# Performance work log

Hardware: AMD Instinct MI355X
Metric: run time of the kernel (lower is better)

Reference implementation:

```python
import jax, jax.numpy as jnp
import numpy as np

KSIZE = 9
SIGMA = 7.0
ALPHA = 0.05
POOL = 7


def _conv(x, w, pad):
    # x: (N, Cin, H, W), w: (Cout, Cin, kh, kw), zero padding, stride 1
    return jax.lax.conv_general_dilated(
        x, w, window_strides=(1, 1), padding=[(pad, pad), (pad, pad)],
        dimension_numbers=("NCHW", "OIHW", "NCHW"))


def setup_inputs() -> dict:
    key = jax.random.key(0)
    x = jax.random.normal(key, (4, 1, 2048, 2048), dtype=jnp.float32)
    # Sobel filters (ImageGradientsLayer): out ch 0 = Ix, out ch 1 = Iy
    sobel_w = jnp.array(
        [[[[-1., 0., 1.], [-2., 0., 2.], [-1., 0., 1.]]],
         [[[-1., -2., -1.], [0., 0., 0.], [1., 2., 1.]]]], dtype=jnp.float32)
    # Normalized 2D Gaussian kernel, ksize=9, sigma=7
    ax = np.arange(KSIZE) - (KSIZE - 1) / 2.0
    g1 = np.exp(-(ax ** 2) / (2.0 * SIGMA ** 2))
    g2 = np.outer(g1, g1)
    g2 = g2 / g2.sum()
    gauss_w = jnp.asarray(g2, dtype=jnp.float32)[None, None]  # (1,1,9,9)
    return {"x": x, "sobel_w": sobel_w, "gauss_w": gauss_w}


def reference(x, sobel_w, gauss_w):
    # 1) ImageGradientsLayer: Sobel conv -> (N, 2, H, W)
    g = _conv(x, sobel_w, 1)
    Ix, Iy = g[:, 0], g[:, 1]
    # 2) ChannelProductLayer: I_xx, I_yy, I_xy -> (N, 3, H, W)
    prods = jnp.stack([Ix * Ix, Iy * Iy, Ix * Iy], axis=1)
    # 3) SecondMomentMatrixLayer: same 9x9 Gaussian on each channel
    N, C, H, W = prods.shape
    S = _conv(prods.reshape(N * C, 1, H, W), gauss_w, (KSIZE - 1) // 2)
    S = S.reshape(N, C, H, W)
    # 4) CornerResponseLayer: R = det - alpha * trace^2
    det = S[:, 0] * S[:, 1] - S[:, 2] * S[:, 2]
    tr = S[:, 0] + S[:, 1]
    R = (det - ALPHA * tr * tr)[:, None]  # (N, 1, H, W)
    # 5) NMSLayer: global (lower) median threshold, 7x7 maxpool, equality mask
    n = R.size
    med = jnp.sort(R.reshape(-1))[(n - 1) // 2]  # torch.median = lower median
    xt = jnp.where(R > med, R, jnp.zeros_like(R))
    pad = (POOL - 1) // 2
    y = jax.lax.reduce_window(
        xt, -jnp.inf, jax.lax.max, (1, 1, POOL, POOL), (1, 1, 1, 1),
        [(0, 0), (0, 0), (pad, pad), (pad, pad)])
    mask = (xt == y).astype(xt.dtype)
    return mask * xt
```

## Files before the change

kernel.cpp:

```cpp
#include <hip/hip_runtime.h>
#include <cstdint>
#include <math.h>

#define IMH 2048
#define IMW 2048
#define NB 4
#define NPIX (NB*IMH*IMW)
#define MEDRANK ((NPIX-1)/2)
#define ALPHA 0.05f

#define TW 64
#define TH 32

__device__ __forceinline__ uint32_t fkey(float f){
  uint32_t u = __float_as_uint(f);
  return (u & 0x80000000u) ? ~u : (u | 0x80000000u);
}

__device__ __forceinline__ float ldz(const float* __restrict__ p, int r, int c){
  return (r >= 0 && r < IMH && c >= 0 && c < IMW) ? p[(size_t)r*IMW + c] : 0.f;
}

__global__ __launch_bounds__(256) void front_kernel(
    const float* __restrict__ x, const float* __restrict__ sobel_w,
    const float* __restrict__ gauss_w, float* __restrict__ R)
{
  __shared__ float xs[TH+10][84];
  __shared__ float hs[3][TH+8][68];

  const int tid = threadIdx.x;
  const int C0 = blockIdx.x * TW;
  const int R0 = blockIdx.y * TH;
  const int n  = blockIdx.z;
  const float* xb = x + (size_t)n * (size_t)(IMH*IMW);

  float w0[9], w1[9];
#pragma unroll
  for (int i = 0; i < 9; i++){ w0[i] = sobel_w[i]; w1[i] = sobel_w[9+i]; }
  float ga[9];
  {
    float a4 = sqrtf(gauss_w[4*9+4]);
#pragma unroll
    for (int i = 0; i < 9; i++) ga[i] = gauss_w[4*9+i] / a4;
  }

  for (int u = tid; u < (TH+10)*20; u += 256){
    int r  = u / 20, c4 = u % 20;
    int gr = R0 - 5 + r;
    int gc = C0 - 8 + c4*4;
    float4 v;
    if (gr >= 0 && gr < IMH && gc >= 0 && gc + 3 < IMW){
      v = *reinterpret_cast<const float4*>(&xb[(size_t)gr*IMW + gc]);
    } else {
      v.x = ldz(xb, gr, gc+0);
      v.y = ldz(xb, gr, gc+1);
      v.z = ldz(xb, gr, gc+2);
      v.w = ldz(xb, gr, gc+3);
    }
    *reinterpret_cast<float4*>(&xs[r][c4*4]) = v;
  }
  __syncthreads();

  for (int u = tid; u < (TH+8)*16; u += 256){
    int hr = u >> 4;
    int oc = (u & 15) * 4;
    int gr = R0 - 4 + hr;
    bool rowv = ((unsigned)gr < (unsigned)IMH);

    float ix[12], iy[12];
#pragma unroll
    for (int j = 0; j < 12; j++){ ix[j] = 0.f; iy[j] = 0.f; }
#pragma unroll
    for (int i = 0; i < 3; i++){
      float xr[20];
#pragma unroll
      for (int m = 0; m < 5; m++){
        float4 t = *reinterpret_cast<const float4*>(&xs[hr+i][oc + m*4]);
        xr[m*4+0]=t.x; xr[m*4+1]=t.y; xr[m*4+2]=t.z; xr[m*4+3]=t.w;
      }
#pragma unroll
      for (int j = 0; j < 12; j++){
#pragma unroll
        for (int d = 0; d < 3; d++){
          float xv = xr[3 + j + d];
          ix[j] = fmaf(w0[i*3+d], xv, ix[j]);
          iy[j] = fmaf(w1[i*3+d], xv, iy[j]);
        }
      }
    }
    float pr[3][12];
#pragma unroll
    for (int j = 0; j < 12; j++){
      int gc = C0 + oc - 4 + j;
      bool v = rowv && ((unsigned)gc < (unsigned)IMW);
      float a = v ? ix[j] : 0.f;
      float b = v ? iy[j] : 0.f;
      pr[0][j] = a*a; pr[1][j] = b*b; pr[2][j] = a*b;
    }
#pragma unroll
    for (int p = 0; p < 3; p++){
      float o[4];
#pragma unroll
      for (int jj = 0; jj < 4; jj++){
        float s = 0.f;
#pragma unroll
        for (int k = 0; k < 9; k++) s = fmaf(ga[k], pr[p][jj+k], s);
        o[jj] = s;
      }
      *reinterpret_cast<float4*>(&hs[p][hr][oc]) = make_float4(o[0],o[1],o[2],o[3]);
    }
  }
  __syncthreads();

  const int c4o = tid & 15;
  const int r0o = (tid >> 4) * 2;
  float4 sA[3], sB[3];
#pragma unroll
  for (int p = 0; p < 3; p++){
    float4 a0 = make_float4(0,0,0,0), a1 = make_float4(0,0,0,0);
#pragma unroll
    for (int k = 0; k < 10; k++){
      float4 hv = *reinterpret_cast<const float4*>(&hs[p][r0o+k][c4o*4]);
      if (k < 9){
        a0.x = fmaf(ga[k], hv.x, a0.x); a0.y = fmaf(ga[k], hv.y, a0.y);
        a0.z = fmaf(ga[k], hv.z, a0.z); a0.w = fmaf(ga[k], hv.w, a0.w);
      }
      if (k >= 1){
        a1.x = fmaf(ga[k-1], hv.x, a1.x); a1.y = fmaf(ga[k-1], hv.y, a1.y);
        a1.z = fmaf(ga[k-1], hv.z, a1.z); a1.w = fmaf(ga[k-1], hv.w, a1.w);
      }
    }
    sA[p] = a0; sB[p] = a1;
  }

  float* Rb = R + (size_t)n * (size_t)(IMH*IMW);
  {
    float4 o0, o1;
    float s0, s1, s2, det, tr;
    s0=sA[0].x; s1=sA[1].x; s2=sA[2].x; det=s0*s1-s2*s2; tr=s0+s1; o0.x=det-ALPHA*tr*tr;
    s0=sA[0].y; s1=sA[1].y; s2=sA[2].y; det=s0*s1-s2*s2; tr=s0+s1; o0.y=det-ALPHA*tr*tr;
    s0=sA[0].z; s1=sA[1].z; s2=sA[2].z; det=s0*s1-s2*s2; tr=s0+s1; o0.z=det-ALPHA*tr*tr;
    s0=sA[0].w; s1=sA[1].w; s2=sA[2].w; det=s0*s1-s2*s2; tr=s0+s1; o0.w=det-ALPHA*tr*tr;
    s0=sB[0].x; s1=sB[1].x; s2=sB[2].x; det=s0*s1-s2*s2; tr=s0+s1; o1.x=det-ALPHA*tr*tr;
    s0=sB[0].y; s1=sB[1].y; s2=sB[2].y; det=s0*s1-s2*s2; tr=s0+s1; o1.y=det-ALPHA*tr*tr;
    s0=sB[0].z; s1=sB[1].z; s2=sB[2].z; det=s0*s1-s2*s2; tr=s0+s1; o1.z=det-ALPHA*tr*tr;
    s0=sB[0].w; s1=sB[1].w; s2=sB[2].w; det=s0*s1-s2*s2; tr=s0+s1; o1.w=det-ALPHA*tr*tr;

    int orow = R0 + r0o;
    int ocol = C0 + c4o*4;
    *reinterpret_cast<float4*>(&Rb[(size_t)orow*IMW + ocol])     = o0;
    *reinterpret_cast<float4*>(&Rb[(size_t)(orow+1)*IMW + ocol]) = o1;
  }
}

__global__ __launch_bounds__(256) void hist8_kernel(
    const float4* __restrict__ R4, uint32_t* __restrict__ h)
{
  __shared__ uint32_t lh[256*32];
  for (int i = threadIdx.x; i < 256*32; i += 256) lh[i] = 0;
  __syncthreads();
  const int copy = threadIdx.x & 31;
  const int stride = gridDim.x * 256;
  for (int i = blockIdx.x*256 + threadIdx.x; i < NPIX/4; i += stride){
    float4 v = R4[i];
    atomicAdd(&lh[(fkey(v.x) >> 24)*32 + copy], 1u);
    atomicAdd(&lh[(fkey(v.y) >> 24)*32 + copy], 1u);
    atomicAdd(&lh[(fkey(v.z) >> 24)*32 + copy], 1u);
    atomicAdd(&lh[(fkey(v.w) >> 24)*32 + copy], 1u);
  }
  __syncthreads();
  {
    const int t = threadIdx.x;
    uint32_t s = 0;
#pragma unroll
    for (int i = 0; i < 32; i++) s += lh[t*32 + ((t + i) & 31)];
    if (s) atomicAdd(&h[t], s);
  }
}

__global__ __launch_bounds__(256) void hist12_kernel(
    const float4* __restrict__ R4, uint32_t* __restrict__ h,
    const uint32_t* __restrict__ state, int phase)
{
  __shared__ uint32_t lh[4096];
  for (int i = threadIdx.x; i < 4096; i += 256) lh[i] = 0;
  __syncthreads();
  const uint32_t target = (phase == 0) ? state[0] : ((state[0] << 12) | state[2]);
  const int shift = (phase == 0) ? 24 : 12;
  const int stride = gridDim.x * 256;
  for (int i = blockIdx.x*256 + threadIdx.x; i < NPIX/4; i += stride){
    float4 v = R4[i];
    uint32_t k;
    k = fkey(v.x); if ((k >> shift) == target) atomicAdd(&lh[(k >> (shift-12)) & 0xfffu], 1u);
    k = fkey(v.y); if ((k >> shift) == target) atomicAdd(&lh[(k >> (shift-12)) & 0xfffu], 1u);
    k = fkey(v.z); if ((k >> shift) == target) atomicAdd(&lh[(k >> (shift-12)) & 0xfffu], 1u);
    k = fkey(v.w); if ((k >> shift) == target) atomicAdd(&lh[(k >> (shift-12)) & 0xfffu], 1u);
  }
  __syncthreads();
  for (int i = threadIdx.x; i < 4096; i += 256)
    if (lh[i]) atomicAdd(&h[i], lh[i]);
}

__global__ __launch_bounds__(256) void select_kernel(
    const uint32_t* __restrict__ h, uint32_t* __restrict__ state,
    int nbins, int phase)
{
  __shared__ uint32_t sc[256];
  const int t = threadIdx.x;
  const int chunk = nbins >> 8;
  uint32_t lsum = 0;
  for (int i = 0; i < chunk; i++) lsum += h[t*chunk + i];
  sc[t] = lsum;
  __syncthreads();
  for (int off = 1; off < 256; off <<= 1){
    uint32_t v = (t >= off) ? sc[t-off] : 0u;
    __syncthreads();
    sc[t] += v;
    __syncthreads();
  }
  const uint32_t excl = sc[t] - lsum;
  const uint32_t rank = (phase == 0) ? (uint32_t)MEDRANK : state[(phase == 1) ? 1 : 3];
  if (rank >= excl && rank < excl + lsum){
    uint32_t cum = excl;
    for (int i = 0; i < chunk; i++){
      uint32_t c = h[t*chunk + i];
      if (rank < cum + c){
        uint32_t bin = (uint32_t)(t*chunk + i);
        if (phase == 0){ state[0] = bin; state[1] = rank - cum; }
        else if (phase == 1){ state[2] = bin; state[3] = rank - cum; }
        else {
          uint32_t key = (state[0] << 24) | (state[2] << 12) | bin;
          uint32_t u = (key & 0x80000000u) ? (key & 0x7fffffffu) : ~key;
          state[4] = u;
        }
        break;
      }
      cum += c;
    }
  }
}

#define PT 64
__global__ __launch_bounds__(256) void nms_kernel(
    const float* __restrict__ R, const uint32_t* __restrict__ state,
    float* __restrict__ out)
{
  __shared__ float xt[PT+6][76];
  __shared__ float hm[PT+6][68];

  const int tid = threadIdx.x;
  const int C0 = blockIdx.x * PT;
  const int R0 = blockIdx.y * PT;
  const int n  = blockIdx.z;
  const float med = __uint_as_float(state[4]);
  const float* Rb = R + (size_t)n * (size_t)(IMH*IMW);

  for (int u = tid; u < 70*18; u += 256){
    int r  = u / 18, c4 = u % 18;
    int gr = R0 - 3 + r;
    int gc = C0 - 4 + c4*4;
    float4 v;
    if (gr >= 0 && gr < IMH && gc >= 0 && gc + 3 < IMW){
      v = *reinterpret_cast<const float4*>(&Rb[(size_t)gr*IMW + gc]);
      v.x = v.x > med ? v.x : 0.f;
      v.y = v.y > med ? v.y : 0.f;
      v.z = v.z > med ? v.z : 0.f;
      v.w = v.w > med ? v.w : 0.f;
    } else {
      float t0, t1, t2, t3;
      t0 = (gr>=0&&gr<IMH&&gc+0>=0&&gc+0<IMW) ? Rb[(size_t)gr*IMW+gc+0] : -INFINITY;
      t1 = (gr>=0&&gr<IMH&&gc+1>=0&&gc+1<IMW) ? Rb[(size_t)gr*IMW+gc+1] : -INFINITY;
      t2 = (gr>=0&&gr<IMH&&gc+2>=0&&gc+2<IMW) ? Rb[(size_t)gr*IMW+gc+2] : -INFINITY;
      t3 = (gr>=0&&gr<IMH&&gc+3>=0&&gc+3<IMW) ? Rb[(size_t)gr*IMW+gc+3] : -INFINITY;
      v.x = (t0 == -INFINITY) ? t0 : (t0 > med ? t0 : 0.f);
      v.y = (t1 == -INFINITY) ? t1 : (t1 > med ? t1 : 0.f);
      v.z = (t2 == -INFINITY) ? t2 : (t2 > med ? t2 : 0.f);
      v.w = (t3 == -INFINITY) ? t3 : (t3 > med ? t3 : 0.f);
    }
    *reinterpret_cast<float4*>(&xt[r][c4*4]) = v;
  }
  __syncthreads();

  for (int u = tid; u < 70*16; u += 256){
    int r = u / 16, c4 = u % 16;
    float4 t0 = *reinterpret_cast<const float4*>(&xt[r][c4*4]);
    float4 t1 = *reinterpret_cast<const float4*>(&xt[r][c4*4+4]);
    float4 t2 = *reinterpret_cast<const float4*>(&xt[r][c4*4+8]);
    float w[12];
    w[0]=t0.x; w[1]=t0.y; w[2]=t0.z; w[3]=t0.w;
    w[4]=t1.x; w[5]=t1.y; w[6]=t1.z; w[7]=t1.w;
    w[8]=t2.x; w[9]=t2.y; w[10]=t2.z; w[11]=t2.w;
    float o[4];
#pragma unroll
    for (int j = 0; j < 4; j++){
      float m = w[j+1];
#pragma unroll
      for (int k = 2; k <= 7; k++) m = fmaxf(m, w[j+k]);
      o[j] = m;
    }
    *reinterpret_cast<float4*>(&hm[r][c4*4]) = make_float4(o[0],o[1],o[2],o[3]);
  }
  __syncthreads();

  const int c4o = tid & 15;
  const int r0o = (tid >> 4) * 4;
  float4 hv[10];
#pragma unroll
  for (int k = 0; k < 10; k++)
    hv[k] = *reinterpret_cast<const float4*>(&hm[r0o+k][c4o*4]);

  float* ob = out + (size_t)n * (size_t)(IMH*IMW);
#pragma unroll
  for (int i = 0; i < 4; i++){
    float4 y = hv[i];
#pragma unroll
    for (int k = 1; k < 7; k++){
      float4 t = hv[i+k];
      y.x = fmaxf(y.x, t.x); y.y = fmaxf(y.y, t.y);
      y.z = fmaxf(y.z, t.z); y.w = fmaxf(y.w, t.w);
    }
    float4 c = *reinterpret_cast<const float4*>(&xt[r0o+i+3][c4o*4+4]);
    float4 o;
    o.x = (c.x == y.x) ? c.x : 0.f;
    o.y = (c.y == y.y) ? c.y : 0.f;
    o.z = (c.z == y.z) ? c.z : 0.f;
    o.w = (c.w == y.w) ? c.w : 0.f;
    *reinterpret_cast<float4*>(&ob[(size_t)(R0+r0o+i)*IMW + C0 + c4o*4]) = o;
  }
}

extern "C" void kernel_launch(void* const* d_in, const int* in_sizes, int n_in,
                              void* d_out, int out_size, void* d_ws, size_t ws_size,
                              hipStream_t stream)
{
  (void)in_sizes; (void)n_in; (void)out_size; (void)ws_size;
  const float* x  = (const float*)d_in[0];
  const float* sw = (const float*)d_in[1];
  const float* gw = (const float*)d_in[2];
  float* out = (float*)d_out;

  float* R = (float*)d_ws;
  uint32_t* hist = (uint32_t*)((char*)d_ws + (size_t)NPIX * sizeof(float));
  uint32_t* h8    = hist;
  uint32_t* h12a  = hist + 256;
  uint32_t* h12b  = hist + 256 + 4096;
  uint32_t* state = hist + 256 + 4096 + 4096;

  hipMemsetAsync(hist, 0, (256 + 4096 + 4096) * sizeof(uint32_t), stream);

  front_kernel<<<dim3(IMW/TW, IMH/TH, NB), 256, 0, stream>>>(x, sw, gw, R);

  hist8_kernel <<<1024, 256, 0, stream>>>((const float4*)R, h8);
  select_kernel<<<1,    256, 0, stream>>>(h8, state, 256, 0);
  hist12_kernel<<<1024, 256, 0, stream>>>((const float4*)R, h12a, state, 0);
  select_kernel<<<1,    256, 0, stream>>>(h12a, state, 4096, 1);
  hist12_kernel<<<1024, 256, 0, stream>>>((const float4*)R, h12b, state, 1);
  select_kernel<<<1,    256, 0, stream>>>(h12b, state, 4096, 2);

  nms_kernel<<<dim3(IMW/PT, IMH/PT, NB), 256, 0, stream>>>(R, state, out);
}
```

Measured before the change: 303.6 us.

## Fold median select into histogram kernels and use separable Sobel with smaller tiles

```diff
diff --git a/kernel.cpp b/kernel.cpp
--- a/kernel.cpp
+++ b/kernel.cpp
@@ -10,23 +10,29 @@
 #define ALPHA 0.05f
 
 #define TW 64
-#define TH 32
+#define TH 24
+#define XROWS (TH+10)
+#define XSTR 84
+#define HROWS (TH+8)
+#define HSTR 68
 
 __device__ __forceinline__ uint32_t fkey(float f){
   uint32_t u = __float_as_uint(f);
   return (u & 0x80000000u) ? ~u : (u | 0x80000000u);
 }
-
+__device__ __forceinline__ uint32_t aload(const uint32_t* p){
+  return __hip_atomic_load(p, __ATOMIC_RELAXED, __HIP_MEMORY_SCOPE_AGENT);
+}
 __device__ __forceinline__ float ldz(const float* __restrict__ p, int r, int c){
   return (r >= 0 && r < IMH && c >= 0 && c < IMW) ? p[(size_t)r*IMW + c] : 0.f;
 }
 
-__global__ __launch_bounds__(256) void front_kernel(
-    const float* __restrict__ x, const float* __restrict__ sobel_w,
-    const float* __restrict__ gauss_w, float* __restrict__ R)
-{
-  __shared__ float xs[TH+10][84];
-  __shared__ float hs[3][TH+8][68];
+__global__ __launch_bounds__(256, 4) void harris_front(
+    const float* __restrict__ x, const float* __restrict__ gauss_w,
+    float* __restrict__ R)
+{
+  __shared__ float xs[XROWS][XSTR];
+  __shared__ float hs[3][HROWS][HSTR];
 
   const int tid = threadIdx.x;
   const int C0 = blockIdx.x * TW;
@@ -34,9 +40,6 @@
   const int n  = blockIdx.z;
   const float* xb = x + (size_t)n * (size_t)(IMH*IMW);
 
-  float w0[9], w1[9];
-#pragma unroll
-  for (int i = 0; i < 9; i++){ w0[i] = sobel_w[i]; w1[i] = sobel_w[9+i]; }
   float ga[9];
   {
     float a4 = sqrtf(gauss_w[4*9+4]);
@@ -44,97 +47,90 @@
     for (int i = 0; i < 9; i++) ga[i] = gauss_w[4*9+i] / a4;
   }
 
-  for (int u = tid; u < (TH+10)*20; u += 256){
-    int r  = u / 20, c4 = u % 20;
+  for (int u = tid; u < XROWS*20; u += 256){
+    int r = u / 20, c4 = u % 20;
     int gr = R0 - 5 + r;
     int gc = C0 - 8 + c4*4;
     float4 v;
     if (gr >= 0 && gr < IMH && gc >= 0 && gc + 3 < IMW){
       v = *reinterpret_cast<const float4*>(&xb[(size_t)gr*IMW + gc]);
     } else {
-      v.x = ldz(xb, gr, gc+0);
-      v.y = ldz(xb, gr, gc+1);
-      v.z = ldz(xb, gr, gc+2);
-      v.w = ldz(xb, gr, gc+3);
+      v.x = ldz(xb, gr, gc+0); v.y = ldz(xb, gr, gc+1);
+      v.z = ldz(xb, gr, gc+2); v.w = ldz(xb, gr, gc+3);
     }
     *reinterpret_cast<float4*>(&xs[r][c4*4]) = v;
   }
   __syncthreads();
 
-  for (int u = tid; u < (TH+8)*16; u += 256){
-    int hr = u >> 4;
-    int oc = (u & 15) * 4;
-    int gr = R0 - 4 + hr;
-    bool rowv = ((unsigned)gr < (unsigned)IMH);
-
-    float ix[12], iy[12];
-#pragma unroll
-    for (int j = 0; j < 12; j++){ ix[j] = 0.f; iy[j] = 0.f; }
-#pragma unroll
-    for (int i = 0; i < 3; i++){
-      float xr[20];
-#pragma unroll
-      for (int m = 0; m < 5; m++){
-        float4 t = *reinterpret_cast<const float4*>(&xs[hr+i][oc + m*4]);
-        xr[m*4+0]=t.x; xr[m*4+1]=t.y; xr[m*4+2]=t.z; xr[m*4+3]=t.w;
+  {
+    const int hr = tid >> 3;
+    const int oc = (tid & 7) * 8;
+    const int gr = R0 - 4 + hr;
+    const bool rowv = ((unsigned)gr < (unsigned)IMH);
+
+    float sv[24], dv[24];
+#pragma unroll
+    for (int m = 0; m < 6; m++){
+      float4 a = *reinterpret_cast<const float4*>(&xs[hr  ][oc + m*4]);
+      float4 b = *reinterpret_cast<const float4*>(&xs[hr+1][oc + m*4]);
+      float4 c = *reinterpret_cast<const float4*>(&xs[hr+2][oc + m*4]);
+      sv[m*4+0] = fmaf(2.f, b.x, a.x + c.x);  dv[m*4+0] = c.x - a.x;
+      sv[m*4+1] = fmaf(2.f, b.y, a.y + c.y);  dv[m*4+1] = c.y - a.y;
+      sv[m*4+2] = fmaf(2.f, b.z, a.z + c.z);  dv[m*4+2] = c.z - a.z;
+      sv[m*4+3] = fmaf(2.f, b.w, a.w + c.w);  dv[m*4+3] = c.w - a.w;
+    }
+    float ix[16], iy[16];
+#pragma unroll
+    for (int j = 0; j < 16; j++){
+      float vx = sv[j+5] - sv[j+3];
+      float vy = dv[j+3] + fmaf(2.f, dv[j+4], dv[j+5]);
+      int gc = C0 + oc - 4 + j;
+      bool vld = rowv && ((unsigned)gc < (unsigned)IMW);
+      ix[j] = vld ? vx : 0.f;
+      iy[j] = vld ? vy : 0.f;
+    }
+#pragma unroll
+    for (int p = 0; p < 3; p++){
+      float pr[16];
+#pragma unroll
+      for (int j = 0; j < 16; j++)
+        pr[j] = (p == 0) ? ix[j]*ix[j] : (p == 1) ? iy[j]*iy[j] : ix[j]*iy[j];
+      float o[8];
+#pragma unroll
+      for (int t2 = 0; t2 < 8; t2++){
+        float s = 0.f;
+#pragma unroll
+        for (int k = 0; k < 9; k++) s = fmaf(ga[k], pr[t2+k], s);
+        o[t2] = s;
       }
-#pragma unroll
-      for (int j = 0; j < 12; j++){
-#pragma unroll
-        for (int d = 0; d < 3; d++){
-          float xv = xr[3 + j + d];
-          ix[j] = fmaf(w0[i*3+d], xv, ix[j]);
-          iy[j] = fmaf(w1[i*3+d], xv, iy[j]);
+      *reinterpret_cast<float4*>(&hs[p][hr][oc])   = make_float4(o[0],o[1],o[2],o[3]);
+      *reinterpret_cast<float4*>(&hs[p][hr][oc+4]) = make_float4(o[4],o[5],o[6],o[7]);
+    }
+  }
+  __syncthreads();
+
+  if (tid < 192){
+    const int c4o = tid & 15;
+    const int r0o = (tid >> 4) * 2;
+    float4 sA[3], sB[3];
+#pragma unroll
+    for (int p = 0; p < 3; p++){
+      float4 a0 = make_float4(0,0,0,0), a1 = make_float4(0,0,0,0);
+#pragma unroll
+      for (int k = 0; k < 10; k++){
+        float4 hv = *reinterpret_cast<const float4*>(&hs[p][r0o+k][c4o*4]);
+        if (k < 9){
+          a0.x = fmaf(ga[k], hv.x, a0.x); a0.y = fmaf(ga[k], hv.y, a0.y);
+          a0.z = fmaf(ga[k], hv.z, a0.z); a0.w = fmaf(ga[k], hv.w, a0.w);
+        }
+        if (k >= 1){
+          a1.x = fmaf(ga[k-1], hv.x, a1.x); a1.y = fmaf(ga[k-1], hv.y, a1.y);
+          a1.z = fmaf(ga[k-1], hv.z, a1.z); a1.w = fmaf(ga[k-1], hv.w, a1.w);
         }
       }
-    }
-    float pr[3][12];
-#pragma unroll
-    for (int j = 0; j < 12; j++){
-      int gc = C0 + oc - 4 + j;
-      bool v = rowv && ((unsigned)gc < (unsigned)IMW);
-      float a = v ? ix[j] : 0.f;
-      float b = v ? iy[j] : 0.f;
-      pr[0][j] = a*a; pr[1][j] = b*b; pr[2][j] = a*b;
-    }
-#pragma unroll
-    for (int p = 0; p < 3; p++){
-      float o[4];
-#pragma unroll
-      for (int jj = 0; jj < 4; jj++){
-        float s = 0.f;
-#pragma unroll
-        for (int k = 0; k < 9; k++) s = fmaf(ga[k], pr[p][jj+k], s);
-        o[jj] = s;
-      }
-      *reinterpret_cast<float4*>(&hs[p][hr][oc]) = make_float4(o[0],o[1],o[2],o[3]);
-    }
-  }
-  __syncthreads();
-
-  const int c4o = tid & 15;
-  const int r0o = (tid >> 4) * 2;
-  float4 sA[3], sB[3];
-#pragma unroll
-  for (int p = 0; p < 3; p++){
-    float4 a0 = make_float4(0,0,0,0), a1 = make_float4(0,0,0,0);
-#pragma unroll
-    for (int k = 0; k < 10; k++){
-      float4 hv = *reinterpret_cast<const float4*>(&hs[p][r0o+k][c4o*4]);
-      if (k < 9){
-        a0.x = fmaf(ga[k], hv.x, a0.x); a0.y = fmaf(ga[k], hv.y, a0.y);
-        a0.z = fmaf(ga[k], hv.z, a0.z); a0.w = fmaf(ga[k], hv.w, a0.w);
-      }
-      if (k >= 1){
-        a1.x = fmaf(ga[k-1], hv.x, a1.x); a1.y = fmaf(ga[k-1], hv.y, a1.y);
-        a1.z = fmaf(ga[k-1], hv.z, a1.z); a1.w = fmaf(ga[k-1], hv.w, a1.w);
-      }
-    }
-    sA[p] = a0; sB[p] = a1;
-  }
-
-  float* Rb = R + (size_t)n * (size_t)(IMH*IMW);
-  {
+      sA[p] = a0; sB[p] = a1;
+    }
+    float* Rb = R + (size_t)n * (size_t)(IMH*IMW);
     float4 o0, o1;
     float s0, s1, s2, det, tr;
     s0=sA[0].x; s1=sA[1].x; s2=sA[2].x; det=s0*s1-s2*s2; tr=s0+s1; o0.x=det-ALPHA*tr*tr;
@@ -146,43 +142,74 @@
     s0=sB[0].z; s1=sB[1].z; s2=sB[2].z; det=s0*s1-s2*s2; tr=s0+s1; o1.z=det-ALPHA*tr*tr;
     s0=sB[0].w; s1=sB[1].w; s2=sB[2].w; det=s0*s1-s2*s2; tr=s0+s1; o1.w=det-ALPHA*tr*tr;
 
-    int orow = R0 + r0o;
-    int ocol = C0 + c4o*4;
-    *reinterpret_cast<float4*>(&Rb[(size_t)orow*IMW + ocol])     = o0;
-    *reinterpret_cast<float4*>(&Rb[(size_t)(orow+1)*IMW + ocol]) = o1;
-  }
-}
-
-__global__ __launch_bounds__(256) void hist8_kernel(
-    const float4* __restrict__ R4, uint32_t* __restrict__ h)
-{
-  __shared__ uint32_t lh[256*32];
-  for (int i = threadIdx.x; i < 256*32; i += 256) lh[i] = 0;
-  __syncthreads();
-  const int copy = threadIdx.x & 31;
+    const int orow = R0 + r0o;
+    const int ocol = C0 + c4o*4;
+    if (orow < IMH)
+      *reinterpret_cast<float4*>(&Rb[(size_t)orow*IMW + ocol]) = o0;
+    if (orow + 1 < IMH)
+      *reinterpret_cast<float4*>(&Rb[(size_t)(orow+1)*IMW + ocol]) = o1;
+  }
+}
+
+#define HREP 32
+__global__ __launch_bounds__(256) void harris_hist8(
+    const float4* __restrict__ R4, uint32_t* __restrict__ h8,
+    uint32_t* __restrict__ state, uint32_t* __restrict__ ctr)
+{
+  __shared__ uint32_t lh[256*HREP];
+  __shared__ uint32_t sc[256];
+  __shared__ int lastFlag;
+  for (int i = threadIdx.x; i < 256*HREP; i += 256) lh[i] = 0;
+  __syncthreads();
+  const int copy = threadIdx.x & (HREP-1);
   const int stride = gridDim.x * 256;
   for (int i = blockIdx.x*256 + threadIdx.x; i < NPIX/4; i += stride){
     float4 v = R4[i];
-    atomicAdd(&lh[(fkey(v.x) >> 24)*32 + copy], 1u);
-    atomicAdd(&lh[(fkey(v.y) >> 24)*32 + copy], 1u);
-    atomicAdd(&lh[(fkey(v.z) >> 24)*32 + copy], 1u);
-    atomicAdd(&lh[(fkey(v.w) >> 24)*32 + copy], 1u);
+    atomicAdd(&lh[(fkey(v.x) >> 24)*HREP + copy], 1u);
+    atomicAdd(&lh[(fkey(v.y) >> 24)*HREP + copy], 1u);
+    atomicAdd(&lh[(fkey(v.z) >> 24)*HREP + copy], 1u);
+    atomicAdd(&lh[(fkey(v.w) >> 24)*HREP + copy], 1u);
   }
   __syncthreads();
   {
     const int t = threadIdx.x;
     uint32_t s = 0;
 #pragma unroll
-    for (int i = 0; i < 32; i++) s += lh[t*32 + ((t + i) & 31)];
-    if (s) atomicAdd(&h[t], s);
-  }
-}
-
-__global__ __launch_bounds__(256) void hist12_kernel(
+    for (int i = 0; i < HREP; i++) s += lh[t*HREP + ((t + i) & (HREP-1))];
+    if (s) atomicAdd(&h8[t], s);
+  }
+  __syncthreads();
+  if (threadIdx.x == 0){
+    __threadfence();
+    lastFlag = (atomicAdd(ctr, 1u) == (uint32_t)gridDim.x - 1u);
+  }
+  __syncthreads();
+  if (!lastFlag) return;
+  __threadfence();
+  const int t = threadIdx.x;
+  uint32_t cnt = aload(&h8[t]);
+  sc[t] = cnt;
+  __syncthreads();
+  for (int off = 1; off < 256; off <<= 1){
+    uint32_t v = (t >= off) ? sc[t-off] : 0u;
+    __syncthreads();
+    sc[t] += v;
+    __syncthreads();
+  }
+  uint32_t excl = sc[t] - cnt;
+  if ((uint32_t)MEDRANK >= excl && (uint32_t)MEDRANK < excl + cnt){
+    state[0] = (uint32_t)t;
+    state[1] = (uint32_t)MEDRANK - excl;
+  }
+}
+
+__global__ __launch_bounds__(256) void harris_hist12(
     const float4* __restrict__ R4, uint32_t* __restrict__ h,
-    const uint32_t* __restrict__ state, int phase)
+    uint32_t* __restrict__ state, uint32_t* __restrict__ ctr, int phase)
 {
   __shared__ uint32_t lh[4096];
+  __shared__ uint32_t sc[256];
+  __shared__ int lastFlag;
   for (int i = threadIdx.x; i < 4096; i += 256) lh[i] = 0;
   __syncthreads();
   const uint32_t target = (phase == 0) ? state[0] : ((state[0] << 12) | state[2]);
@@ -199,17 +226,19 @@
   __syncthreads();
   for (int i = threadIdx.x; i < 4096; i += 256)
     if (lh[i]) atomicAdd(&h[i], lh[i]);
-}
-
-__global__ __launch_bounds__(256) void select_kernel(
-    const uint32_t* __restrict__ h, uint32_t* __restrict__ state,
-    int nbins, int phase)
-{
-  __shared__ uint32_t sc[256];
+  __syncthreads();
+  if (threadIdx.x == 0){
+    __threadfence();
+    lastFlag = (atomicAdd(ctr, 1u) == (uint32_t)gridDim.x - 1u);
+  }
+  __syncthreads();
+  if (!lastFlag) return;
+  __threadfence();
   const int t = threadIdx.x;
-  const int chunk = nbins >> 8;
+  uint32_t vals[16];
   uint32_t lsum = 0;
-  for (int i = 0; i < chunk; i++) lsum += h[t*chunk + i];
+#pragma unroll
+  for (int i = 0; i < 16; i++){ vals[i] = aload(&h[t*16 + i]); lsum += vals[i]; }
   sc[t] = lsum;
   __syncthreads();
   for (int off = 1; off < 256; off <<= 1){
@@ -218,16 +247,14 @@
     sc[t] += v;
     __syncthreads();
   }
-  const uint32_t excl = sc[t] - lsum;
-  const uint32_t rank = (phase == 0) ? (uint32_t)MEDRANK : state[(phase == 1) ? 1 : 3];
+  uint32_t excl = sc[t] - lsum;
+  uint32_t rank = (phase == 0) ? state[1] : state[3];
   if (rank >= excl && rank < excl + lsum){
     uint32_t cum = excl;
-    for (int i = 0; i < chunk; i++){
-      uint32_t c = h[t*chunk + i];
-      if (rank < cum + c){
-        uint32_t bin = (uint32_t)(t*chunk + i);
-        if (phase == 0){ state[0] = bin; state[1] = rank - cum; }
-        else if (phase == 1){ state[2] = bin; state[3] = rank - cum; }
+    for (int i = 0; i < 16; i++){
+      if (rank < cum + vals[i]){
+        uint32_t bin = (uint32_t)(t*16 + i);
+        if (phase == 0){ state[2] = bin; state[3] = rank - cum; }
         else {
           uint32_t key = (state[0] << 24) | (state[2] << 12) | bin;
           uint32_t u = (key & 0x80000000u) ? (key & 0x7fffffffu) : ~key;
@@ -235,13 +262,13 @@
         }
         break;
       }
-      cum += c;
+      cum += vals[i];
     }
   }
 }
 
 #define PT 64
-__global__ __launch_bounds__(256) void nms_kernel(
+__global__ __launch_bounds__(256) void harris_nms(
     const float* __restrict__ R, const uint32_t* __restrict__ state,
     float* __restrict__ out)
 {
@@ -335,27 +362,24 @@
 {
   (void)in_sizes; (void)n_in; (void)out_size; (void)ws_size;
   const float* x  = (const float*)d_in[0];
-  const float* sw = (const float*)d_in[1];
   const float* gw = (const float*)d_in[2];
   float* out = (float*)d_out;
 
   float* R = (float*)d_ws;
-  uint32_t* hist = (uint32_t*)((char*)d_ws + (size_t)NPIX * sizeof(float));
+  uint32_t* hist  = (uint32_t*)((char*)d_ws + (size_t)NPIX * sizeof(float));
   uint32_t* h8    = hist;
   uint32_t* h12a  = hist + 256;
   uint32_t* h12b  = hist + 256 + 4096;
   uint32_t* state = hist + 256 + 4096 + 4096;
-
-  hipMemsetAsync(hist, 0, (256 + 4096 + 4096) * sizeof(uint32_t), stream);
-
-  front_kernel<<<dim3(IMW/TW, IMH/TH, NB), 256, 0, stream>>>(x, sw, gw, R);
-
-  hist8_kernel <<<1024, 256, 0, stream>>>((const float4*)R, h8);
-  select_kernel<<<1,    256, 0, stream>>>(h8, state, 256, 0);
-  hist12_kernel<<<1024, 256, 0, stream>>>((const float4*)R, h12a, state, 0);
-  select_kernel<<<1,    256, 0, stream>>>(h12a, state, 4096, 1);
-  hist12_kernel<<<1024, 256, 0, stream>>>((const float4*)R, h12b, state, 1);
-  select_kernel<<<1,    256, 0, stream>>>(h12b, state, 4096, 2);
-
-  nms_kernel<<<dim3(IMW/PT, IMH/PT, NB), 256, 0, stream>>>(R, state, out);
-}
+  uint32_t* ctr   = state + 8;
+
+  hipMemsetAsync(hist, 0, (256 + 4096 + 4096 + 8 + 3) * sizeof(uint32_t), stream);
+
+  harris_front<<<dim3(IMW/TW, (IMH + TH - 1)/TH, NB), 256, 0, stream>>>(x, gw, R);
+
+  harris_hist8 <<<1024, 256, 0, stream>>>((const float4*)R, h8, state, ctr);
+  harris_hist12<<<1024, 256, 0, stream>>>((const float4*)R, h12a, state, ctr+1, 0);
+  harris_hist12<<<1024, 256, 0, stream>>>((const float4*)R, h12b, state, ctr+2, 1);
+
+  harris_nms<<<dim3(IMW/PT, IMH/PT, NB), 256, 0, stream>>>(R, state, out);
+}
```

After: 419.7 us. 38.2% more time.
